# Kernel tuning notes

Measured on AMD Instinct MI355X. Metric: run time of the kernel, lower is better.

Reference implementation:

```python
import jax, jax.numpy as jnp
import numpy as np


def gcn_layer(x, W, b, src, dst):
    """PyG GCNConv with improved=True: A_hat = A + 2I, D^-1/2 A_hat D^-1/2 X W + b."""
    n = x.shape[0]
    xw = x @ W  # [N, H]
    # degree counts each incoming edge (weight 1) plus self-loop weight 2
    deg = jnp.zeros((n,), x.dtype).at[dst].add(jnp.ones((src.shape[0],), x.dtype)) + 2.0
    dinv = jax.lax.rsqrt(deg)  # deg >= 2 always
    norm = (dinv[src] * dinv[dst])[:, None]  # [E, 1]
    agg = jax.ops.segment_sum(xw[src] * norm, dst, num_segments=n)  # scatter-add to dst
    agg = agg + (2.0 * dinv * dinv)[:, None] * xw  # self-loop contribution (weight 2)
    return agg + b


def xavier(k, shape):
    lim = (6.0 / (shape[0] + shape[1])) ** 0.5
    return jax.random.uniform(k, shape, jnp.float32, -lim, lim)


def setup_inputs() -> dict:
    key = jax.random.key(0)
    ks = jax.random.split(key, 8)
    N, E, D = 100_000, 1_600_000, 64  # nodes, edges, features_dim
    H1, H2 = 64, 64                   # gnn_dims
    M1, M2 = 128, 64                  # ind_pol_dims
    rep = jax.random.normal(ks[0], (N, D), jnp.float32)
    edge_index = jax.random.randint(ks[1], (2, E), 0, N, jnp.int32)
    return {
        "rep": rep,
        "edge_index": edge_index,
        "W1": xavier(ks[2], (D, H1)), "b1": jnp.zeros((H1,), jnp.float32),
        "W2": xavier(ks[3], (H1, H2)), "b2": jnp.zeros((H2,), jnp.float32),
        "Wa": xavier(ks[4], (H2 + D, M1)), "ba": jnp.zeros((M1,), jnp.float32),
        "Wb": xavier(ks[5], (M1, M2)), "bb": jnp.zeros((M2,), jnp.float32),
        "Wo": xavier(ks[6], (M2, 1)), "bo": jnp.zeros((1,), jnp.float32),
    }


def reference(rep, edge_index, W1, b1, W2, b2, Wa, ba, Wb, bb, Wo, bo):
    src, dst = edge_index[0], edge_index[1]
    # eval mode: f.dropout(training=False) is identity
    h = jax.nn.relu(gcn_layer(rep, W1, b1, src, dst))
    h = jax.nn.relu(gcn_layer(h, W2, b2, src, dst))
    z = jnp.concatenate([rep, h], axis=1)  # [N, D + H2]
    z = jax.nn.relu(z @ Wa + ba)
    z = jax.nn.relu(z @ Wb + bb)
    prob = jax.nn.sigmoid(z @ Wo + bo)[:, 0]  # [N]
    # gumbel_softmax(hard=True, tau=1) over logits = [1-p, p] (torch semantics:
    # probabilities fed directly as logits, as in the original code)
    logits = jnp.stack([1.0 - prob, prob], axis=1)  # [N, 2]
    u = jax.random.uniform(jax.random.key(42), logits.shape, jnp.float32, 1e-20, 1.0)
    g = -jnp.log(-jnp.log(u))
    y = jax.nn.softmax(logits + g, axis=1)
    hard = jax.nn.one_hot(jnp.argmax(y, axis=1), 2, dtype=y.dtype)
    st = hard + y - jax.lax.stop_gradient(y)  # straight-through
    ind = st @ jnp.array([[0.0], [1.0]], dtype=y.dtype)  # mm with [[0],[1]]
    return (prob, ind[:, 0])
```

## Files before the change

### kernel.cpp

```cpp
#include <hip/hip_runtime.h>
#include <math.h>


__device__ __forceinline__ unsigned rotl32(unsigned x, int r) {
  return (x << r) | (x >> (32 - r));
}

__device__ __forceinline__ void threefry2x32(unsigned k0, unsigned k1,
                                             unsigned x0, unsigned x1,
                                             unsigned& o0, unsigned& o1) {
  unsigned ks2 = k0 ^ k1 ^ 0x1BD11BDAu;
#define TF_RND(r) { x0 += x1; x1 = rotl32(x1, (r)); x1 ^= x0; }
  x0 += k0; x1 += k1;
  TF_RND(13) TF_RND(15) TF_RND(26) TF_RND(6)
  x0 += k1; x1 += ks2 + 1u;
  TF_RND(17) TF_RND(29) TF_RND(16) TF_RND(24)
  x0 += ks2; x1 += k0 + 2u;
  TF_RND(13) TF_RND(15) TF_RND(26) TF_RND(6)
  x0 += k0; x1 += k1 + 3u;
  TF_RND(17) TF_RND(29) TF_RND(16) TF_RND(24)
  x0 += k1; x1 += ks2 + 4u;
  TF_RND(13) TF_RND(15) TF_RND(26) TF_RND(6)
  x0 += ks2; x1 += k0 + 5u;
#undef TF_RND
  o0 = x0; o1 = x1;
}

__device__ __forceinline__ unsigned jax_random_bits_u32(unsigned k0, unsigned k1,
                                                        unsigned flat_idx) {
  unsigned a, b;
  threefry2x32(k0, k1, 0u, flat_idx, a, b);
  return a ^ b;
}

#define BSHIFT 8
#define BMASK 255

__global__ __launch_bounds__(256) void coarse_hist_kernel(
    const int* __restrict__ dst, int* __restrict__ coarse, int E) {
  __shared__ int h[512];
  for (int i = threadIdx.x; i < 512; i += 256) h[i] = 0;
  __syncthreads();
  for (int e = blockIdx.x * blockDim.x + threadIdx.x; e < E;
       e += gridDim.x * blockDim.x)
    atomicAdd(&h[dst[e] >> BSHIFT], 1);
  __syncthreads();
  for (int i = threadIdx.x; i < 512; i += 256)
    if (h[i]) atomicAdd(&coarse[i], h[i]);
}

__global__ __launch_bounds__(512) void coarse_scan_kernel(
    const int* __restrict__ coarse, int* __restrict__ bbase,
    int* __restrict__ cbase, int NBUCK) {
  __shared__ int sh[512];
  int t = threadIdx.x;
  int v = (t < NBUCK) ? coarse[t] : 0;
  sh[t] = v;
  __syncthreads();
  for (int o = 1; o < 512; o <<= 1) {
    int a = (t >= o) ? sh[t - o] : 0;
    __syncthreads();
    sh[t] += a;
    __syncthreads();
  }
  if (t < NBUCK) {
    int ex = sh[t] - v;
    bbase[t] = ex;
    cbase[t] = ex;
    if (t == NBUCK - 1) bbase[NBUCK] = sh[t];
  }
}

#define CHUNK 4096
__global__ __launch_bounds__(256) void bucket_scatter_kernel(
    const int* __restrict__ src, const int* __restrict__ dst,
    int* __restrict__ cbase, int* __restrict__ pkB, int E) {
  __shared__ int sS[CHUNK];
  __shared__ int dS[CHUNK];
  __shared__ int cnt[512];
  __shared__ int base[512];
  const int t = threadIdx.x;
  const int e0 = blockIdx.x * CHUNK;
  const int n = min(CHUNK, E - e0);
  for (int i = t; i < 512; i += 256) cnt[i] = 0;
  for (int i = t; i < n; i += 256) {
    sS[i] = src[e0 + i];
    dS[i] = dst[e0 + i];
  }
  __syncthreads();
  for (int i = t; i < n; i += 256) atomicAdd(&cnt[dS[i] >> BSHIFT], 1);
  __syncthreads();
  for (int i = t; i < 512; i += 256) {
    int c = cnt[i];
    base[i] = c ? atomicAdd(&cbase[i], c) : 0;
  }
  __syncthreads();
  for (int i = t; i < 512; i += 256) cnt[i] = 0;
  __syncthreads();
  for (int i = t; i < n; i += 256) {
    int d = dS[i];
    int b = d >> BSHIFT;
    int r = atomicAdd(&cnt[b], 1);
    pkB[base[b] + r] = ((d & BMASK) << 20) | sS[i];
  }
}

__global__ __launch_bounds__(256) void bucket_finalize_kernel(
    const int* __restrict__ pkB, const int* __restrict__ bbase,
    int* __restrict__ off, float* __restrict__ dinv, int* __restrict__ srcS,
    int N) {
  __shared__ int cnt[256];
  __shared__ int sh[256];
  const int t = threadIdx.x;
  const int b = blockIdx.x;
  const int lo = bbase[b], hi = bbase[b + 1];
  cnt[t] = 0;
  __syncthreads();
  for (int i = lo + t; i < hi; i += 256) atomicAdd(&cnt[pkB[i] >> 20], 1);
  __syncthreads();
  const int deg = cnt[t];
  sh[t] = deg;
  __syncthreads();
  for (int o = 1; o < 256; o <<= 1) {
    int a = (t >= o) ? sh[t - o] : 0;
    __syncthreads();
    sh[t] += a;
    __syncthreads();
  }
  const int ex = sh[t] - deg;
  const int node = (b << BSHIFT) + t;
  if (node < N) {
    off[node] = lo + ex;
    dinv[node] = 1.0f / sqrtf((float)deg + 2.0f);
    if (node == N - 1) off[N] = hi;
  }
  cnt[t] = lo + ex;
  __syncthreads();
  for (int i = lo + t; i < hi; i += 256) {
    int u = pkB[i];
    int pos = atomicAdd(&cnt[u >> 20], 1);
    srcS[pos] = u & 0xFFFFF;
  }
}

__global__ __launch_bounds__(256) void aggregate_kernel(
    const float* __restrict__ xws, const int* __restrict__ srcS,
    const int* __restrict__ off, const float* __restrict__ dinv,
    const float* __restrict__ bias, float* __restrict__ h, int N) {
  int node = (blockIdx.x * blockDim.x + threadIdx.x) >> 6;
  int lane = threadIdx.x & 63;
  int g = lane >> 4;
  int fq = lane & 15;
  if (node >= N) return;
  const float4* xw4 = (const float4*)xws;
  int beg = off[node], end = off[node + 1];
  float4 a0 = make_float4(0.f, 0.f, 0.f, 0.f);
  float4 a1 = a0, a2 = a0, a3 = a0;
  int e = beg;
  for (; e + 16 <= end; e += 16) {
    int s0 = srcS[e + g];
    int s1 = srcS[e + 4 + g];
    int s2 = srcS[e + 8 + g];
    int s3 = srcS[e + 12 + g];
    float4 v0 = xw4[(size_t)s0 * 16 + fq];
    float4 v1 = xw4[(size_t)s1 * 16 + fq];
    float4 v2 = xw4[(size_t)s2 * 16 + fq];
    float4 v3 = xw4[(size_t)s3 * 16 + fq];
    a0.x += v0.x; a0.y += v0.y; a0.z += v0.z; a0.w += v0.w;
    a1.x += v1.x; a1.y += v1.y; a1.z += v1.z; a1.w += v1.w;
    a2.x += v2.x; a2.y += v2.y; a2.z += v2.z; a2.w += v2.w;
    a3.x += v3.x; a3.y += v3.y; a3.z += v3.z; a3.w += v3.w;
  }
  for (; e < end; e += 4) {
    if (e + g < end) {
      float4 v = xw4[(size_t)srcS[e + g] * 16 + fq];
      a0.x += v.x; a0.y += v.y; a0.z += v.z; a0.w += v.w;
    }
  }
  float4 a;
  a.x = (a0.x + a1.x) + (a2.x + a3.x);
  a.y = (a0.y + a1.y) + (a2.y + a3.y);
  a.z = (a0.z + a1.z) + (a2.z + a3.z);
  a.w = (a0.w + a1.w) + (a2.w + a3.w);
  a.x += __shfl_xor(a.x, 16, 64); a.x += __shfl_xor(a.x, 32, 64);
  a.y += __shfl_xor(a.y, 16, 64); a.y += __shfl_xor(a.y, 32, 64);
  a.z += __shfl_xor(a.z, 16, 64); a.z += __shfl_xor(a.z, 32, 64);
  a.w += __shfl_xor(a.w, 16, 64); a.w += __shfl_xor(a.w, 32, 64);
  if (g == 0) {
    float di = dinv[node];
    float4 self = xw4[(size_t)node * 16 + fq];
    float4 b = ((const float4*)bias)[fq];
    float4 r;
    r.x = fmaxf(di * (a.x + 2.0f * self.x) + b.x, 0.f);
    r.y = fmaxf(di * (a.y + 2.0f * self.y) + b.y, 0.f);
    r.z = fmaxf(di * (a.z + 2.0f * self.z) + b.z, 0.f);
    r.w = fmaxf(di * (a.w + 2.0f * self.w) + b.w, 0.f);
    *(float4*)&h[(size_t)node * 64 + fq * 4] = r;
  }
}

__global__ __launch_bounds__(256) void gemm64v2_kernel(
    const float* __restrict__ X, const float* __restrict__ W,
    const float* __restrict__ dinv, float* __restrict__ Y, int N, int flags) {
  __shared__ float Ws[64 * 64];
  __shared__ float Xs[64 * 68];
  const int t = threadIdx.x;
  {
    const float4* W4 = (const float4*)W;
    float4* Ws4 = (float4*)Ws;
    for (int i = t; i < 16 * 64; i += 256) Ws4[i] = W4[i];
  }
  const int row0 = blockIdx.x * 64;
  for (int i = t; i < 64 * 16; i += 256) {
    int r = i >> 4, c4 = i & 15;
    int gr = row0 + r;
    float4 v = make_float4(0.f, 0.f, 0.f, 0.f);
    if (gr < N) v = *(const float4*)&X[(size_t)gr * 64 + c4 * 4];
    *(float4*)&Xs[r * 68 + c4 * 4] = v;
  }
  __syncthreads();

  const int tx = t & 15, ty = t >> 4;
  const int c0 = tx * 4;
  const int r0 = ty * 4;
  float acc[4][4];
#pragma unroll
  for (int i = 0; i < 4; ++i)
#pragma unroll
    for (int j = 0; j < 4; ++j) acc[i][j] = 0.f;

#pragma unroll 4
  for (int k4 = 0; k4 < 16; ++k4) {
    float4 xv[4];
#pragma unroll
    for (int i = 0; i < 4; ++i)
      xv[i] = *(const float4*)&Xs[(r0 + i) * 68 + k4 * 4];
#pragma unroll
    for (int kk = 0; kk < 4; ++kk) {
      float w[4];
#pragma unroll
      for (int j = 0; j < 4; ++j) w[j] = Ws[(k4 * 4 + kk) * 64 + c0 + j];
      const float xk[4] = {
          kk == 0 ? xv[0].x : kk == 1 ? xv[0].y : kk == 2 ? xv[0].z : xv[0].w,
          kk == 0 ? xv[1].x : kk == 1 ? xv[1].y : kk == 2 ? xv[1].z : xv[1].w,
          kk == 0 ? xv[2].x : kk == 1 ? xv[2].y : kk == 2 ? xv[2].z : xv[2].w,
          kk == 0 ? xv[3].x : kk == 1 ? xv[3].y : kk == 2 ? xv[3].z : xv[3].w};
#pragma unroll
      for (int i = 0; i < 4; ++i)
#pragma unroll
        for (int j = 0; j < 4; ++j) acc[i][j] = fmaf(xk[i], w[j], acc[i][j]);
    }
  }

#pragma unroll
  for (int i = 0; i < 4; ++i) {
    int gr = row0 + r0 + i;
    if (gr >= N) continue;
    float sc = (flags & 8) ? dinv[gr] : 1.0f;
    float4 v = make_float4(acc[i][0], acc[i][1], acc[i][2], acc[i][3]);
    if (flags & 8) { v.x *= sc; v.y *= sc; v.z *= sc; v.w *= sc; }
    *(float4*)&Y[(size_t)gr * 64 + c0] = v;
  }
}

__global__ __launch_bounds__(256) void head_mega_kernel(
    const float* __restrict__ rep, const float* __restrict__ h2,
    const float* __restrict__ Wa, const float* __restrict__ ba,
    const float* __restrict__ Wb, const float* __restrict__ bb,
    const float* __restrict__ Wo, const float* __restrict__ bo,
    float* __restrict__ out, int N) {
  __shared__ float Xs[64 * 128];
  __shared__ float Wbuf[32 * 128];
  const int t = threadIdx.x;
  const int row0 = blockIdx.x * 64;

  for (int i = t; i < 2048; i += 256) {
    int r = i >> 5, c4 = i & 31;
    int gr = row0 + r;
    float4 v = make_float4(0.f, 0.f, 0.f, 0.f);
    if (gr < N)
      v = (c4 < 16) ? *(const float4*)&rep[(size_t)gr * 64 + c4 * 4]
                    : *(const float4*)&h2[(size_t)gr * 64 + (c4 - 16) * 4];
    int scol = (c4 * 4 + ((r >> 2) << 2)) & 127;
    *(float4*)&Xs[r * 128 + scol] = v;
  }

  const int tx = t & 15, ty = t >> 4;
  const int cL = tx * 4;
  const int cH = 64 + tx * 4;
  const int r0 = ty * 4;
  float za[4][8];
#pragma unroll
  for (int i = 0; i < 4; ++i)
#pragma unroll
    for (int j = 0; j < 8; ++j) za[i][j] = 0.f;

  for (int chunk = 0; chunk < 4; ++chunk) {
    __syncthreads();
    const float4* Wa4 = (const float4*)(Wa + chunk * 32 * 128);
    float4* Wd = (float4*)Wbuf;
    for (int i = t; i < 1024; i += 256) Wd[i] = Wa4[i];
    __syncthreads();
    const int kb = chunk * 32;
#pragma unroll 2
    for (int kk = 0; kk < 32; ++kk) {
      const int kc = (kb + kk + (ty << 2)) & 127;
      float x[4];
#pragma unroll
      for (int i = 0; i < 4; ++i) x[i] = Xs[(r0 + i) * 128 + kc];
      float4 w0 = *(const float4*)&Wbuf[kk * 128 + cL];
      float4 w1 = *(const float4*)&Wbuf[kk * 128 + cH];
      const float w[8] = {w0.x, w0.y, w0.z, w0.w, w1.x, w1.y, w1.z, w1.w};
#pragma unroll
      for (int i = 0; i < 4; ++i)
#pragma unroll
        for (int j = 0; j < 8; ++j) za[i][j] = fmaf(x[i], w[j], za[i][j]);
    }
  }
#pragma unroll
  for (int i = 0; i < 4; ++i) {
#pragma unroll
    for (int j = 0; j < 4; ++j) {
      za[i][j] = fmaxf(za[i][j] + ba[cL + j], 0.f);
      za[i][4 + j] = fmaxf(za[i][4 + j] + ba[cH + j], 0.f);
    }
  }

  __syncthreads();
  float* zaS = Xs;
  {
    int sL = (cL + (ty << 2)) & 127;
    int sH = (cH + (ty << 2)) & 127;
#pragma unroll
    for (int i = 0; i < 4; ++i) {
      *(float4*)&zaS[(r0 + i) * 128 + sL] =
          make_float4(za[i][0], za[i][1], za[i][2], za[i][3]);
      *(float4*)&zaS[(r0 + i) * 128 + sH] =
          make_float4(za[i][4], za[i][5], za[i][6], za[i][7]);
    }
  }

  const int c0b = tx * 4;
  float zb[4][4];
#pragma unroll
  for (int i = 0; i < 4; ++i)
#pragma unroll
    for (int j = 0; j < 4; ++j) zb[i][j] = 0.f;

  for (int chunk = 0; chunk < 2; ++chunk) {
    __syncthreads();
    const float4* Wb4 = (const float4*)(Wb + chunk * 64 * 64);
    float4* Wd = (float4*)Wbuf;
    for (int i = t; i < 1024; i += 256) Wd[i] = Wb4[i];
    __syncthreads();
    const int kb = chunk * 64;
#pragma unroll 4
    for (int kk = 0; kk < 64; ++kk) {
      const int kc = (kb + kk + (ty << 2)) & 127;
      float x[4];
#pragma unroll
      for (int i = 0; i < 4; ++i) x[i] = zaS[(r0 + i) * 128 + kc];
      float4 w = *(const float4*)&Wbuf[kk * 64 + c0b];
      const float wj[4] = {w.x, w.y, w.z, w.w};
#pragma unroll
      for (int i = 0; i < 4; ++i)
#pragma unroll
        for (int j = 0; j < 4; ++j) zb[i][j] = fmaf(x[i], wj[j], zb[i][j]);
    }
  }
  float part[4];
#pragma unroll
  for (int i = 0; i < 4; ++i) {
    part[i] = 0.f;
#pragma unroll
    for (int j = 0; j < 4; ++j) {
      float v = fmaxf(zb[i][j] + bb[c0b + j], 0.f);
      part[i] = fmaf(v, Wo[c0b + j], part[i]);
    }
  }
  __syncthreads();
  float* red = Wbuf;
#pragma unroll
  for (int i = 0; i < 4; ++i) red[tx * 68 + r0 + i] = part[i];
  __syncthreads();
  if (t < 64) {
    int gr = row0 + t;
    if (gr < N) {
      float s = 0.f;
#pragma unroll
      for (int u = 0; u < 16; ++u) s += red[u * 68 + t];
      float w = s + bo[0];
      float p = 1.0f / (1.0f + expf(-w));
      unsigned i = (unsigned)gr;
      unsigned bits0 = jax_random_bits_u32(0u, 42u, 2u * i);
      unsigned bits1 = jax_random_bits_u32(0u, 42u, 2u * i + 1u);
      float f0 = __uint_as_float((bits0 >> 9) | 0x3f800000u) - 1.0f;
      float f1 = __uint_as_float((bits1 >> 9) | 0x3f800000u) - 1.0f;
      float u0 = fmaxf(1e-20f, f0 + 1e-20f);
      float u1 = fmaxf(1e-20f, f1 + 1e-20f);
      float g0 = -logf(-logf(u0));
      float g1 = -logf(-logf(u1));
      float a0 = (1.0f - p) + g0;
      float a1 = p + g1;
      float m = fmaxf(a0, a1);
      float e0 = expf(a0 - m), e1 = expf(a1 - m);
      float ssum = e0 + e1;
      float y0 = e0 / ssum, y1 = e1 / ssum;
      float hard1 = (y1 > y0) ? 1.0f : 0.0f;
      float st1 = (hard1 + y1) - y1;
      out[gr] = p;
      out[N + gr] = st1;
    }
  }
}

extern "C" void kernel_launch(void* const* d_in, const int* in_sizes, int n_in,
                              void* d_out, int out_size, void* d_ws, size_t ws_size,
                              hipStream_t stream) {
  const float* rep = (const float*)d_in[0];
  const int* ei = (const int*)d_in[1];
  const float* W1 = (const float*)d_in[2];
  const float* b1 = (const float*)d_in[3];
  const float* W2 = (const float*)d_in[4];
  const float* b2 = (const float*)d_in[5];
  const float* Wa = (const float*)d_in[6];
  const float* ba = (const float*)d_in[7];
  const float* Wb = (const float*)d_in[8];
  const float* bb = (const float*)d_in[9];
  const float* Wo = (const float*)d_in[10];
  const float* bo = (const float*)d_in[11];
  float* out = (float*)d_out;

  const int N = in_sizes[0] / 64;
  const int E = in_sizes[1] / 2;
  const int* srcI = ei;
  const int* dstI = ei + E;

  const int NBUCK = (N + 255) >> BSHIFT;

  float* ws = (float*)d_ws;
  float* bufA = ws;
  float* bufB = bufA + (size_t)N * 64;
  float* dinv = bufB + (size_t)N * 64;
  int* coarse = (int*)(dinv + N);
  int* bbase = coarse + 512;
  int* cbase = bbase + 513;
  int* off = cbase + 512;
  int* pkB = off + N + 1;
  int* srcS = pkB + E;

  const int nb64 = (N + 63) / 64;
  const int nbW = (N + 3) / 4;
  const int nbA = (E + CHUNK - 1) / CHUNK;

  hipMemsetAsync(coarse, 0, 512 * 4, stream);
  coarse_hist_kernel<<<256, 256, 0, stream>>>(dstI, coarse, E);
  coarse_scan_kernel<<<1, 512, 0, stream>>>(coarse, bbase, cbase, NBUCK);
  bucket_scatter_kernel<<<nbA, 256, 0, stream>>>(srcI, dstI, cbase, pkB, E);
  bucket_finalize_kernel<<<NBUCK, 256, 0, stream>>>(pkB, bbase, off, dinv,
                                                    srcS, N);

  gemm64v2_kernel<<<nb64, 256, 0, stream>>>(rep, W1, dinv, bufA, N, 8);
  aggregate_kernel<<<nbW, 256, 0, stream>>>(bufA, srcS, off, dinv, b1, bufB, N);

  gemm64v2_kernel<<<nb64, 256, 0, stream>>>(bufB, W2, dinv, bufA, N, 8);
  aggregate_kernel<<<nbW, 256, 0, stream>>>(bufA, srcS, off, dinv, b2, bufB, N);

  head_mega_kernel<<<nb64, 256, 0, stream>>>(rep, bufB, Wa, ba, Wb, bb, Wo, bo,
                                             out, N);
}
```

Baseline: 393.2 us.

## Predicate aggregate tail loads and enlarge head MLP per-thread register tile

The aggregate kernel's remainder loop is folded into the main 16-edge loop: indices are clamped and the accumulation is predicated, so short neighbor lists still issue four independent gathers instead of a serial tail. The head MLP kernel drops to 128 threads per block, each computing an 8-row tile instead of 4, and reads activations from shared memory as float4 along k. This is meant to cut shared-memory load traffic per FMA and improve ILP, at the cost of more registers and fewer threads per block.

After: 419.2 us. 1.07x slower.

```diff
diff --git a/kernel.cpp b/kernel.cpp
--- a/kernel.cpp
+++ b/kernel.cpp
@@ -156,26 +156,20 @@
   int beg = off[node], end = off[node + 1];
   float4 a0 = make_float4(0.f, 0.f, 0.f, 0.f);
   float4 a1 = a0, a2 = a0, a3 = a0;
-  int e = beg;
-  for (; e + 16 <= end; e += 16) {
-    int s0 = srcS[e + g];
-    int s1 = srcS[e + 4 + g];
-    int s2 = srcS[e + 8 + g];
-    int s3 = srcS[e + 12 + g];
+  for (int e = beg; e < end; e += 16) {
+    int e0 = e + g, e1 = e + 4 + g, e2 = e + 8 + g, e3 = e + 12 + g;
+    int s0 = srcS[min(e0, end - 1)];
+    int s1 = srcS[min(e1, end - 1)];
+    int s2 = srcS[min(e2, end - 1)];
+    int s3 = srcS[min(e3, end - 1)];
     float4 v0 = xw4[(size_t)s0 * 16 + fq];
     float4 v1 = xw4[(size_t)s1 * 16 + fq];
     float4 v2 = xw4[(size_t)s2 * 16 + fq];
     float4 v3 = xw4[(size_t)s3 * 16 + fq];
-    a0.x += v0.x; a0.y += v0.y; a0.z += v0.z; a0.w += v0.w;
-    a1.x += v1.x; a1.y += v1.y; a1.z += v1.z; a1.w += v1.w;
-    a2.x += v2.x; a2.y += v2.y; a2.z += v2.z; a2.w += v2.w;
-    a3.x += v3.x; a3.y += v3.y; a3.z += v3.z; a3.w += v3.w;
-  }
-  for (; e < end; e += 4) {
-    if (e + g < end) {
-      float4 v = xw4[(size_t)srcS[e + g] * 16 + fq];
-      a0.x += v.x; a0.y += v.y; a0.z += v.z; a0.w += v.w;
-    }
+    if (e0 < end) { a0.x += v0.x; a0.y += v0.y; a0.z += v0.z; a0.w += v0.w; }
+    if (e1 < end) { a1.x += v1.x; a1.y += v1.y; a1.z += v1.z; a1.w += v1.w; }
+    if (e2 < end) { a2.x += v2.x; a2.y += v2.y; a2.z += v2.z; a2.w += v2.w; }
+    if (e3 < end) { a3.x += v3.x; a3.y += v3.y; a3.z += v3.z; a3.w += v3.w; }
   }
   float4 a;
   a.x = (a0.x + a1.x) + (a2.x + a3.x);
@@ -263,7 +257,7 @@
   }
 }
 
-__global__ __launch_bounds__(256) void head_mega_kernel(
+__global__ __launch_bounds__(128) void head_mega_kernel(
     const float* __restrict__ rep, const float* __restrict__ h2,
     const float* __restrict__ Wa, const float* __restrict__ ba,
     const float* __restrict__ Wb, const float* __restrict__ bb,
@@ -274,7 +268,7 @@
   const int t = threadIdx.x;
   const int row0 = blockIdx.x * 64;
 
-  for (int i = t; i < 2048; i += 256) {
+  for (int i = t; i < 2048; i += 128) {
     int r = i >> 5, c4 = i & 31;
     int gr = row0 + r;
     float4 v = make_float4(0.f, 0.f, 0.f, 0.f);
@@ -288,10 +282,10 @@
   const int tx = t & 15, ty = t >> 4;
   const int cL = tx * 4;
   const int cH = 64 + tx * 4;
-  const int r0 = ty * 4;
-  float za[4][8];
-#pragma unroll
-  for (int i = 0; i < 4; ++i)
+  const int r0 = ty * 8;
+  float za[8][8];
+#pragma unroll
+  for (int i = 0; i < 8; ++i)
 #pragma unroll
     for (int j = 0; j < 8; ++j) za[i][j] = 0.f;
 
@@ -299,26 +293,35 @@
     __syncthreads();
     const float4* Wa4 = (const float4*)(Wa + chunk * 32 * 128);
     float4* Wd = (float4*)Wbuf;
-    for (int i = t; i < 1024; i += 256) Wd[i] = Wa4[i];
+    for (int i = t; i < 1024; i += 128) Wd[i] = Wa4[i];
     __syncthreads();
     const int kb = chunk * 32;
-#pragma unroll 2
-    for (int kk = 0; kk < 32; ++kk) {
-      const int kc = (kb + kk + (ty << 2)) & 127;
-      float x[4];
-#pragma unroll
-      for (int i = 0; i < 4; ++i) x[i] = Xs[(r0 + i) * 128 + kc];
-      float4 w0 = *(const float4*)&Wbuf[kk * 128 + cL];
-      float4 w1 = *(const float4*)&Wbuf[kk * 128 + cH];
-      const float w[8] = {w0.x, w0.y, w0.z, w0.w, w1.x, w1.y, w1.z, w1.w};
-#pragma unroll
-      for (int i = 0; i < 4; ++i)
-#pragma unroll
-        for (int j = 0; j < 8; ++j) za[i][j] = fmaf(x[i], w[j], za[i][j]);
-    }
-  }
-#pragma unroll
-  for (int i = 0; i < 4; ++i) {
+    for (int k4 = 0; k4 < 8; ++k4) {
+      float4 xq[8];
+#pragma unroll
+      for (int i = 0; i < 8; ++i) {
+        int rr = r0 + i;
+        int kc = (kb + k4 * 4 + ((rr >> 2) << 2)) & 127;
+        xq[i] = *(const float4*)&Xs[rr * 128 + kc];
+      }
+#pragma unroll
+      for (int sub = 0; sub < 4; ++sub) {
+        int kk = k4 * 4 + sub;
+        float4 w0 = *(const float4*)&Wbuf[kk * 128 + cL];
+        float4 w1 = *(const float4*)&Wbuf[kk * 128 + cH];
+        const float w[8] = {w0.x, w0.y, w0.z, w0.w, w1.x, w1.y, w1.z, w1.w};
+#pragma unroll
+        for (int i = 0; i < 8; ++i) {
+          float x = sub == 0 ? xq[i].x : sub == 1 ? xq[i].y
+                  : sub == 2 ? xq[i].z : xq[i].w;
+#pragma unroll
+          for (int j = 0; j < 8; ++j) za[i][j] = fmaf(x, w[j], za[i][j]);
+        }
+      }
+    }
+  }
+#pragma unroll
+  for (int i = 0; i < 8; ++i) {
 #pragma unroll
     for (int j = 0; j < 4; ++j) {
       za[i][j] = fmaxf(za[i][j] + ba[cL + j], 0.f);
@@ -328,22 +331,22 @@
 
   __syncthreads();
   float* zaS = Xs;
-  {
-    int sL = (cL + (ty << 2)) & 127;
-    int sH = (cH + (ty << 2)) & 127;
-#pragma unroll
-    for (int i = 0; i < 4; ++i) {
-      *(float4*)&zaS[(r0 + i) * 128 + sL] =
-          make_float4(za[i][0], za[i][1], za[i][2], za[i][3]);
-      *(float4*)&zaS[(r0 + i) * 128 + sH] =
-          make_float4(za[i][4], za[i][5], za[i][6], za[i][7]);
-    }
+#pragma unroll
+  for (int i = 0; i < 8; ++i) {
+    int rr = r0 + i;
+    int sw = (rr >> 2) << 2;
+    int sL = (cL + sw) & 127;
+    int sH = (cH + sw) & 127;
+    *(float4*)&zaS[rr * 128 + sL] =
+        make_float4(za[i][0], za[i][1], za[i][2], za[i][3]);
+    *(float4*)&zaS[rr * 128 + sH] =
+        make_float4(za[i][4], za[i][5], za[i][6], za[i][7]);
   }
 
   const int c0b = tx * 4;
-  float zb[4][4];
-#pragma unroll
-  for (int i = 0; i < 4; ++i)
+  float zb[8][4];
+#pragma unroll
+  for (int i = 0; i < 8; ++i)
 #pragma unroll
     for (int j = 0; j < 4; ++j) zb[i][j] = 0.f;
 
@@ -351,26 +354,35 @@
     __syncthreads();
     const float4* Wb4 = (const float4*)(Wb + chunk * 64 * 64);
     float4* Wd = (float4*)Wbuf;
-    for (int i = t; i < 1024; i += 256) Wd[i] = Wb4[i];
+    for (int i = t; i < 1024; i += 128) Wd[i] = Wb4[i];
     __syncthreads();
     const int kb = chunk * 64;
-#pragma unroll 4
-    for (int kk = 0; kk < 64; ++kk) {
-      const int kc = (kb + kk + (ty << 2)) & 127;
-      float x[4];
-#pragma unroll
-      for (int i = 0; i < 4; ++i) x[i] = zaS[(r0 + i) * 128 + kc];
-      float4 w = *(const float4*)&Wbuf[kk * 64 + c0b];
-      const float wj[4] = {w.x, w.y, w.z, w.w};
-#pragma unroll
-      for (int i = 0; i < 4; ++i)
-#pragma unroll
-        for (int j = 0; j < 4; ++j) zb[i][j] = fmaf(x[i], wj[j], zb[i][j]);
-    }
-  }
-  float part[4];
-#pragma unroll
-  for (int i = 0; i < 4; ++i) {
+    for (int k4 = 0; k4 < 16; ++k4) {
+      float4 xq[8];
+#pragma unroll
+      for (int i = 0; i < 8; ++i) {
+        int rr = r0 + i;
+        int kc = (kb + k4 * 4 + ((rr >> 2) << 2)) & 127;
+        xq[i] = *(const float4*)&zaS[rr * 128 + kc];
+      }
+#pragma unroll
+      for (int sub = 0; sub < 4; ++sub) {
+        int kk = k4 * 4 + sub;
+        float4 w = *(const float4*)&Wbuf[kk * 64 + c0b];
+        const float wj[4] = {w.x, w.y, w.z, w.w};
+#pragma unroll
+        for (int i = 0; i < 8; ++i) {
+          float x = sub == 0 ? xq[i].x : sub == 1 ? xq[i].y
+                  : sub == 2 ? xq[i].z : xq[i].w;
+#pragma unroll
+          for (int j = 0; j < 4; ++j) zb[i][j] = fmaf(x, wj[j], zb[i][j]);
+        }
+      }
+    }
+  }
+  float part[8];
+#pragma unroll
+  for (int i = 0; i < 8; ++i) {
     part[i] = 0.f;
 #pragma unroll
     for (int j = 0; j < 4; ++j) {
@@ -381,7 +393,7 @@
   __syncthreads();
   float* red = Wbuf;
 #pragma unroll
-  for (int i = 0; i < 4; ++i) red[tx * 68 + r0 + i] = part[i];
+  for (int i = 0; i < 8; ++i) red[tx * 68 + r0 + i] = part[i];
   __syncthreads();
   if (t < 64) {
     int gr = row0 + t;
@@ -466,6 +478,6 @@
   gemm64v2_kernel<<<nb64, 256, 0, stream>>>(bufB, W2, dinv, bufA, N, 8);
   aggregate_kernel<<<nbW, 256, 0, stream>>>(bufA, srcS, off, dinv, b2, bufB, N);
 
-  head_mega_kernel<<<nb64, 256, 0, stream>>>(rep, bufB, Wa, ba, Wb, bb, Wo, bo,
+  head_mega_kernel<<<nb64, 128, 0, stream>>>(rep, bufB, Wa, ba, Wb, bb, Wo, bo,
                                              out, N);
 }
```
